# Kernel optimization log

Hardware: AMD Instinct MI355X
Metric: run time of the kernel (lower is better)

Reference implementation:

```python
import jax, jax.numpy as jnp
import numpy as np

NUM_CAMS = 1
NUM_HEADS = 1
NUM_LEVELS = 1
NUM_POINTS = 4
NUM_DEPTH = 128
EMBED = 128  # must equal NUM_DEPTH (output_proj is applied to the depth axis)


def setup_inputs() -> dict:
    key0 = jax.random.key(0)
    ks = jax.random.split(key0, 12)
    bsv, nq, nv = 1, 1024, 1024  # nq == nv == H*W (32*32)
    off_dim = NUM_CAMS * NUM_HEADS * NUM_LEVELS * NUM_DEPTH * NUM_POINTS * 2  # 1024
    aw_dim = NUM_CAMS * NUM_HEADS * NUM_LEVELS * NUM_DEPTH * NUM_POINTS       # 512
    return {
        "query": jax.random.normal(ks[0], (bsv, nq, EMBED), jnp.float32),
        "key": jax.random.normal(ks[1], (NUM_CAMS, nv, bsv, EMBED), jnp.float32),
        "value": jax.random.normal(ks[2], (NUM_CAMS, nv, bsv, EMBED), jnp.float32),
        "ref_3d": jax.random.uniform(ks[3], (bsv * NUM_CAMS, nq * NUM_DEPTH, 2), jnp.float32),
        "spatial_shapes": jnp.array([[32, 32]], dtype=jnp.int32),
        "W_off": jax.random.normal(ks[4], (EMBED, off_dim), jnp.float32) * 0.02,
        "b_off": jax.random.normal(ks[5], (off_dim,), jnp.float32) * 0.02,
        "W_attn": jax.random.normal(ks[6], (EMBED, aw_dim), jnp.float32) * 0.02,
        "b_attn": jax.random.normal(ks[7], (aw_dim,), jnp.float32) * 0.02,
        "W_v": jax.random.normal(ks[8], (EMBED, EMBED), jnp.float32) / np.sqrt(EMBED),
        "b_v": jnp.zeros((EMBED,), jnp.float32),
        "W_o": jax.random.normal(ks[9], (EMBED, EMBED), jnp.float32) / np.sqrt(EMBED),
        "b_o": jnp.zeros((EMBED,), jnp.float32),
    }


def _bilinear_sample(val, H, W, x, y):
    """grid_sample(align_corners=False, padding=zeros) equivalent.
    val: [B, H*W, D]; x, y: [B, Q, P] in pixel coords. Returns [B, Q, P, D]."""
    B, Q, P = x.shape
    D = val.shape[-1]
    x0f = jnp.floor(x); y0f = jnp.floor(y)
    ix0 = x0f.astype(jnp.int32); iy0 = y0f.astype(jnp.int32)
    wx1 = x - x0f; wy1 = y - y0f
    wx0 = 1.0 - wx1; wy0 = 1.0 - wy1

    def corner(ix, iy, w):
        valid = (ix >= 0) & (ix < W) & (iy >= 0) & (iy < H)
        idx = jnp.clip(iy, 0, H - 1) * W + jnp.clip(ix, 0, W - 1)  # [B,Q,P]
        g = jnp.take_along_axis(val, idx.reshape(B, Q * P)[:, :, None], axis=1)
        g = g.reshape(B, Q, P, D)
        return g * (w * valid.astype(val.dtype))[..., None]

    return (corner(ix0, iy0, wx0 * wy0)
            + corner(ix0 + 1, iy0, wx1 * wy0)
            + corner(ix0, iy0 + 1, wx0 * wy1)
            + corner(ix0 + 1, iy0 + 1, wx1 * wy1))


def reference(query, key, value, ref_3d, spatial_shapes,
              W_off, b_off, W_attn, b_attn, W_v, b_v, W_o, b_o):
    bsv, nq, E = query.shape
    cams, nv, bs, _ = key.shape
    identity = query

    # key/value: [cams, nv, bs, E] -> [bsv, nv, E]
    key2 = jnp.transpose(key, (2, 0, 1, 3)).reshape(bsv, nv, E)
    val = jnp.flip(value, axis=0)
    val = jnp.transpose(val, (2, 0, 1, 3)).reshape(bsv, nv, E)
    val = val @ W_v + b_v
    val = val.reshape(bsv * cams, nv, E)  # num_heads=1 -> head_dim=E

    # offsets / attention weights (heads=levels=1 axes squeezed)
    off = (query @ W_off + b_off).reshape(bsv, nq, cams, NUM_DEPTH, NUM_POINTS, 2)
    aw = (query @ W_attn + b_attn).reshape(bsv, nq, cams, NUM_DEPTH, NUM_LEVELS * NUM_POINTS)
    aw = jax.nn.softmax(aw, axis=-1).reshape(bsv, nq, cams, NUM_DEPTH, NUM_POINTS)
    off = jnp.transpose(off, (0, 2, 1, 3, 4, 5)).reshape(bsv * cams, nq * NUM_DEPTH, NUM_POINTS, 2)
    aw = jnp.transpose(aw, (0, 2, 1, 3, 4)).reshape(bsv * cams, nq * NUM_DEPTH, NUM_POINTS)

    H = spatial_shapes[0, 0]
    W = spatial_shapes[0, 1]
    norm = jnp.stack([W, H]).astype(off.dtype)  # [W, H]
    loc = ref_3d[:, :, None, :] + off / norm    # [B, Qe, P, 2] in [0,1]
    x = loc[..., 0] * W.astype(loc.dtype) - 0.5
    y = loc[..., 1] * H.astype(loc.dtype) - 0.5

    sampled = _bilinear_sample(val, H, W, x, y)          # [B, Qe, P, E]
    out = jnp.einsum('bqpe,bqp->bqe', sampled, aw)       # weighted sum over points

    out = out.reshape(bsv, cams, nq, NUM_DEPTH, E).mean(axis=1)  # [bsv, nq, depth, E]
    out = (out * key2[:, :, None, :]).mean(axis=-1)              # [bsv, nq, depth]
    out = out @ W_o + b_o                                        # depth == EMBED
    return out + identity  # dropout = identity in eval
```

## Files before the change

kernel.cpp:

```cpp
#include <hip/hip_runtime.h>


#define NQ   1024
#define NV   1024
#define ND   128
#define NP   4
#define IMG_W 32
#define IMG_H 32
#define QB   4

typedef __attribute__((ext_vector_type(8))) short bfx8;
typedef __attribute__((ext_vector_type(4))) float f32x4;
typedef __attribute__((ext_vector_type(8))) float f32x8;

__device__ __forceinline__ unsigned short bf_rne(float f) {
  unsigned u = __float_as_uint(f);
  return (unsigned short)((u + 0x7FFFu + ((u >> 16) & 1u)) >> 16);
}
__device__ __forceinline__ float bf2f(unsigned short u) {
  return __uint_as_float((unsigned)u << 16);
}
__device__ __forceinline__ bfx8 pack8(const float* p) {
  bfx8 v;
#pragma unroll
  for (int j = 0; j < 8; ++j) v[j] = (short)bf_rne(p[j]);
  return v;
}

__global__ __launch_bounds__(512) void mono_kernel(
    const float* __restrict__ query, const float* __restrict__ key,
    const float* __restrict__ value, const float* __restrict__ ref3d,
    const float* __restrict__ W_off, const float* __restrict__ b_off,
    const float* __restrict__ W_attn, const float* __restrict__ b_attn,
    const float* __restrict__ W_v, const float* __restrict__ b_v,
    const float* __restrict__ W_o, const float* __restrict__ b_o,
    float* __restrict__ out) {
  __shared__ float q_lds[QB][128];
  __shared__ float key_lds[QB][128];
  __shared__ float keyp_lds[QB][128];
  __shared__ float c_lds[QB];
  __shared__ unsigned short img_bf[QB][NV];
  __shared__ unsigned short off_bf[QB][1024];
  __shared__ unsigned short aw_bf[QB][512];
  __shared__ float o1s[QB][128];

  const int tid = threadIdx.x;
  const int q0 = blockIdx.x * QB;
  const int w = tid >> 6, l = tid & 63;
  const int col = l & 15, g = l >> 4;

  if (tid < 128) {
    ((float4*)q_lds)[tid] = ((const float4*)(query + (size_t)q0 * 128))[tid];
  } else if (tid < 256) {
    ((float4*)key_lds)[tid - 128] =
        ((const float4*)(key + (size_t)q0 * 128))[tid - 128];
  }
  __syncthreads();

  {
    bfx8 afK[4];
#pragma unroll
    for (int ks = 0; ks < 4; ++ks) {
      bfx8 a;
      if (col < QB) {
        a = pack8(&key_lds[col][ks * 32 + g * 8]);
      } else {
#pragma unroll
        for (int j = 0; j < 8; ++j) a[j] = 0;
      }
      afK[ks] = a;
    }
    {
      const float* wvp = W_v + (size_t)(w * 16 + col) * 128 + g * 8;
      f32x8 raw[4];
#pragma unroll
      for (int ks = 0; ks < 4; ++ks)
        raw[ks] = *(const f32x8*)(wvp + ks * 32);
      f32x4 acc = {0.f, 0.f, 0.f, 0.f};
#pragma unroll
      for (int ks = 0; ks < 4; ++ks) {
        bfx8 b;
#pragma unroll
        for (int j = 0; j < 8; ++j) b[j] = (short)bf_rne(raw[ks][j]);
        acc = __builtin_amdgcn_mfma_f32_16x16x32_bf16(afK[ks], b, acc,
                                                      0, 0, 0);
      }
      if (g == 0) {
#pragma unroll
        for (int i = 0; i < QB; ++i) keyp_lds[i][w * 16 + col] = acc[i];
      }
    }
    if (tid < QB) {
      float s = 0.f;
      for (int e = 0; e < 128; e += 4) {
        const float4 bv = *(const float4*)(b_v + e);
        const float4 k4 = *(const float4*)(&key_lds[tid][e]);
        s = fmaf(bv.x, k4.x,
            fmaf(bv.y, k4.y, fmaf(bv.z, k4.z, fmaf(bv.w, k4.w, s))));
      }
      c_lds[tid] = s;
    }
  }
  __syncthreads();

  if (w < 4) {
    const int t = tid;
    float4 aoff[QB];
    float2 aaw[QB];
#pragma unroll
    for (int qq = 0; qq < QB; ++qq) {
      aoff[qq] = make_float4(0.f, 0.f, 0.f, 0.f);
      aaw[qq] = make_float2(0.f, 0.f);
    }
    const float* wo_p = W_off + (size_t)t * 4;
    const float* wa_p = W_attn + (size_t)t * 2;
#pragma unroll 8
    for (int e4 = 0; e4 < 32; ++e4) {
      float4 q4[QB];
#pragma unroll
      for (int qq = 0; qq < QB; ++qq)
        q4[qq] = *(const float4*)(&q_lds[qq][e4 * 4]);
#pragma unroll
      for (int j = 0; j < 4; ++j) {
        const int e = e4 * 4 + j;
        const float4 w4 = *(const float4*)(wo_p + (size_t)e * 1024);
        const float2 w2 = *(const float2*)(wa_p + (size_t)e * 512);
#pragma unroll
        for (int qq = 0; qq < QB; ++qq) {
          const float* qp = (const float*)&q4[qq];
          const float qv = qp[j];
          aoff[qq].x = fmaf(qv, w4.x, aoff[qq].x);
          aoff[qq].y = fmaf(qv, w4.y, aoff[qq].y);
          aoff[qq].z = fmaf(qv, w4.z, aoff[qq].z);
          aoff[qq].w = fmaf(qv, w4.w, aoff[qq].w);
          aaw[qq].x = fmaf(qv, w2.x, aaw[qq].x);
          aaw[qq].y = fmaf(qv, w2.y, aaw[qq].y);
        }
      }
    }
    const float4 bo4 = *(const float4*)(b_off + t * 4);
    const float2 ba2 = *(const float2*)(b_attn + t * 2);
#pragma unroll
    for (int qq = 0; qq < QB; ++qq) {
      const unsigned lo = (unsigned)bf_rne(aoff[qq].x + bo4.x) |
                          ((unsigned)bf_rne(aoff[qq].y + bo4.y) << 16);
      const unsigned hi = (unsigned)bf_rne(aoff[qq].z + bo4.z) |
                          ((unsigned)bf_rne(aoff[qq].w + bo4.w) << 16);
      *(uint2*)(&off_bf[qq][t * 4]) = make_uint2(lo, hi);
      *(unsigned*)(&aw_bf[qq][t * 2]) =
          (unsigned)bf_rne(aaw[qq].x + ba2.x) |
          ((unsigned)bf_rne(aaw[qq].y + ba2.y) << 16);
    }
  } else {
    const int ww = w - 4;
    bfx8 afrag[4];
#pragma unroll
    for (int ks = 0; ks < 4; ++ks) {
      bfx8 a;
      if (col < QB) {
        a = pack8(&keyp_lds[col][ks * 32 + g * 8]);
      } else {
#pragma unroll
        for (int j = 0; j < 8; ++j) a[j] = 0;
      }
      afrag[ks] = a;
    }
    float cq[QB];
#pragma unroll
    for (int i = 0; i < QB; ++i) cq[i] = c_lds[i];

    const float* rowp = value + (size_t)(ww * 256 + col) * 128 + g * 8;
#pragma unroll 2
    for (int f = 0; f < 16; ++f) {
      const float* rp = rowp + (size_t)f * 16 * 128;
      f32x8 raw[4];
#pragma unroll
      for (int ks = 0; ks < 4; ++ks)
        raw[ks] = *(const f32x8*)(rp + ks * 32);
      f32x4 acc = {0.f, 0.f, 0.f, 0.f};
#pragma unroll
      for (int ks = 0; ks < 4; ++ks) {
        bfx8 b;
#pragma unroll
        for (int j = 0; j < 8; ++j) b[j] = (short)bf_rne(raw[ks][j]);
        acc = __builtin_amdgcn_mfma_f32_16x16x32_bf16(afrag[ks], b, acc,
                                                      0, 0, 0);
      }
      if (g == 0) {
        const int v = ww * 256 + f * 16 + col;
#pragma unroll
        for (int i = 0; i < QB; ++i)
          img_bf[i][v] = bf_rne(acc[i] + cq[i]);
      }
    }
  }
  __syncthreads();

  {
    const int qq = tid >> 7;
    const int q = q0 + qq;
    const int d = tid & 127;
    const unsigned short* im = img_bf[qq];
    const size_t qe = (size_t)q * ND + d;

    const float rx = ref3d[qe * 2 + 0];
    const float ry = ref3d[qe * 2 + 1];

    const uint2 ua = *(const uint2*)(&aw_bf[qq][d * 4]);
    const float a0 = bf2f((unsigned short)(ua.x & 0xffff));
    const float a1 = bf2f((unsigned short)(ua.x >> 16));
    const float a2 = bf2f((unsigned short)(ua.y & 0xffff));
    const float a3 = bf2f((unsigned short)(ua.y >> 16));
    const float mx = fmaxf(fmaxf(a0, a1), fmaxf(a2, a3));
    const float e0 = __expf(a0 - mx), e1 = __expf(a1 - mx),
                e2 = __expf(a2 - mx), e3 = __expf(a3 - mx);
    const float inv = 1.0f / (e0 + e1 + e2 + e3);
    const float wgt4[4] = {e0 * inv, e1 * inv, e2 * inv, e3 * inv};

    const uint4 uo = *(const uint4*)(&off_bf[qq][d * 8]);
    const unsigned ox[4] = {uo.x, uo.y, uo.z, uo.w};

    float acc = 0.0f;
#pragma unroll
    for (int p = 0; p < NP; ++p) {
      const float x = rx * (float)IMG_W + bf2f((unsigned short)(ox[p] & 0xffff)) - 0.5f;
      const float y = ry * (float)IMG_H + bf2f((unsigned short)(ox[p] >> 16)) - 0.5f;
      const float xf = floorf(x), yf = floorf(y);
      const int ix0 = (int)xf, iy0 = (int)yf;
      const float wx1 = x - xf, wy1 = y - yf;
      const float wx0 = 1.0f - wx1, wy0 = 1.0f - wy1;

      float s = 0.0f;
#pragma unroll
      for (int cy = 0; cy < 2; ++cy) {
#pragma unroll
        for (int cx = 0; cx < 2; ++cx) {
          const int ix = ix0 + cx, iy = iy0 + cy;
          const bool valid = (ix >= 0) & (ix < IMG_W) & (iy >= 0) & (iy < IMG_H);
          const int cix = min(max(ix, 0), IMG_W - 1);
          const int ciy = min(max(iy, 0), IMG_H - 1);
          const float wgt = (cx ? wx1 : wx0) * (cy ? wy1 : wy0);
          s += valid ? bf2f(im[ciy * IMG_W + cix]) * wgt : 0.0f;
        }
      }
      acc += wgt4[p] * s;
    }
    o1s[qq][d] = acc * (1.0f / 128.0f);
  }
  __syncthreads();

  {
    const int qq = tid >> 7;
    const int n = tid & 127;
    float acc = b_o[n] + q_lds[qq][n];
#pragma unroll 8
    for (int d = 0; d < 128; ++d)
      acc = fmaf(o1s[qq][d], W_o[(size_t)d * 128 + n], acc);
    out[(size_t)(q0 + qq) * 128 + n] = acc;
  }
}

extern "C" void kernel_launch(void* const* d_in, const int* in_sizes, int n_in,
                              void* d_out, int out_size, void* d_ws, size_t ws_size,
                              hipStream_t stream) {
  const float* query  = (const float*)d_in[0];
  const float* key    = (const float*)d_in[1];
  const float* value  = (const float*)d_in[2];
  const float* ref3d  = (const float*)d_in[3];
  const float* W_off  = (const float*)d_in[5];
  const float* b_off  = (const float*)d_in[6];
  const float* W_attn = (const float*)d_in[7];
  const float* b_attn = (const float*)d_in[8];
  const float* W_v    = (const float*)d_in[9];
  const float* b_v    = (const float*)d_in[10];
  const float* W_o    = (const float*)d_in[11];
  const float* b_o    = (const float*)d_in[12];
  float* out = (float*)d_out;

  mono_kernel<<<NQ / QB, 512, 0, stream>>>(query, key, value, ref3d,
                                           W_off, b_off, W_attn, b_attn,
                                           W_v, b_v, W_o, b_o, out);
}
```

Before: 121.3 us.

## Pre-convert value and W_v to swizzled bf16 workspace and software-pipeline loads

A new prep kernel converts value and W_v to bf16 once per call into a workspace with an XOR-swizzled row layout. The main kernel then reads half-size bf16 fragments directly instead of loading fp32 and converting in every block, which removes 256x redundant conversion work and halves global traffic. The offset/attention projection and value-projection loops are also software-pipelined with double-buffered register loads, and launch bounds now request two blocks per CU. The cost is an extra kernel launch and workspace round trip, plus higher register pressure from the double buffers.

```diff
diff --git a/kernel.cpp b/kernel.cpp
--- a/kernel.cpp
+++ b/kernel.cpp
@@ -1,4 +1,5 @@
 #include <hip/hip_runtime.h>
+#include <hip/hip_bf16.h>
 
 
 #define NQ   1024
@@ -9,13 +10,16 @@
 #define IMG_H 32
 #define QB   4
 
+#define WS_VAL 0
+#define WS_WV  262144
+
 typedef __attribute__((ext_vector_type(8))) short bfx8;
 typedef __attribute__((ext_vector_type(4))) float f32x4;
-typedef __attribute__((ext_vector_type(8))) float f32x8;
 
 __device__ __forceinline__ unsigned short bf_rne(float f) {
-  unsigned u = __float_as_uint(f);
-  return (unsigned short)((u + 0x7FFFu + ((u >> 16) & 1u)) >> 16);
+  union { __hip_bfloat16 h; unsigned short u; } v;
+  v.h = __float2bfloat16(f);
+  return v.u;
 }
 __device__ __forceinline__ float bf2f(unsigned short u) {
   return __uint_as_float((unsigned)u << 16);
@@ -27,14 +31,83 @@
   return v;
 }
 
-__global__ __launch_bounds__(512) void mono_kernel(
+__global__ __launch_bounds__(256) void prep_kernel(
+    const float* __restrict__ value, const float* __restrict__ W_v,
+    char* __restrict__ ws) {
+  const int idx = blockIdx.x * 256 + threadIdx.x;
+  if (idx < 16384) {
+    const int row = idx >> 4, cc = idx & 15;
+    const bfx8 v = pack8(value + (size_t)row * 128 + cc * 8);
+    *(bfx8*)(ws + WS_VAL + row * 256 + ((cc * 16) ^ ((row & 15) << 4))) = v;
+  } else if (idx < 18432) {
+    const int j = idx - 16384;
+    const int row = j >> 4, cc = j & 15;
+    const bfx8 v = pack8(W_v + (size_t)row * 128 + cc * 8);
+    *(bfx8*)(ws + WS_WV + row * 256 + ((cc * 16) ^ ((row & 15) << 4))) = v;
+  }
+}
+
+#define SLOAD(WO, WA, bb)                                                \
+  _Pragma("unroll") for (int j_ = 0; j_ < 4; ++j_) {                     \
+    WO[j_] = *(const float4*)(wo_p + (size_t)((bb) * 4 + j_) * 1024);    \
+    WA[j_] = *(const float2*)(wa_p + (size_t)((bb) * 4 + j_) * 512);     \
+  }
+
+#define SFMA(WO, WA, bb)                                                 \
+  _Pragma("unroll") for (int j_ = 0; j_ < 4; ++j_) {                     \
+    const int e_ = (bb) * 4 + j_;                                        \
+    _Pragma("unroll") for (int qq_ = 0; qq_ < QB; ++qq_) {               \
+      const float qv_ = q_lds[qq_][e_];                                  \
+      aoff[qq_].x = fmaf(qv_, WO[j_].x, aoff[qq_].x);                    \
+      aoff[qq_].y = fmaf(qv_, WO[j_].y, aoff[qq_].y);                    \
+      aoff[qq_].z = fmaf(qv_, WO[j_].z, aoff[qq_].z);                    \
+      aoff[qq_].w = fmaf(qv_, WO[j_].w, aoff[qq_].w);                    \
+      aaw[qq_].x = fmaf(qv_, WA[j_].x, aaw[qq_].x);                      \
+      aaw[qq_].y = fmaf(qv_, WA[j_].y, aaw[qq_].y);                      \
+    }                                                                    \
+  }
+
+#define VLOAD(D, s_)                                                     \
+  {                                                                      \
+    const char* p_ = lanep + (size_t)(s_) * 8192;                        \
+    D[0] = *(const bfx8*)(p_ + cb0);                                     \
+    D[1] = *(const bfx8*)(p_ + cb1);                                     \
+    D[2] = *(const bfx8*)(p_ + cb2);                                     \
+    D[3] = *(const bfx8*)(p_ + cb3);                                     \
+    D[4] = *(const bfx8*)(p_ + 4096 + cb0);                              \
+    D[5] = *(const bfx8*)(p_ + 4096 + cb1);                              \
+    D[6] = *(const bfx8*)(p_ + 4096 + cb2);                              \
+    D[7] = *(const bfx8*)(p_ + 4096 + cb3);                              \
+  }
+
+#define VCOMP(S, s_)                                                     \
+  {                                                                      \
+    f32x4 a0_ = {0.f, 0.f, 0.f, 0.f}, a1_ = {0.f, 0.f, 0.f, 0.f};       \
+    a0_ = __builtin_amdgcn_mfma_f32_16x16x32_bf16(afrag[0], S[0], a0_, 0, 0, 0); \
+    a0_ = __builtin_amdgcn_mfma_f32_16x16x32_bf16(afrag[1], S[1], a0_, 0, 0, 0); \
+    a0_ = __builtin_amdgcn_mfma_f32_16x16x32_bf16(afrag[2], S[2], a0_, 0, 0, 0); \
+    a0_ = __builtin_amdgcn_mfma_f32_16x16x32_bf16(afrag[3], S[3], a0_, 0, 0, 0); \
+    a1_ = __builtin_amdgcn_mfma_f32_16x16x32_bf16(afrag[0], S[4], a1_, 0, 0, 0); \
+    a1_ = __builtin_amdgcn_mfma_f32_16x16x32_bf16(afrag[1], S[5], a1_, 0, 0, 0); \
+    a1_ = __builtin_amdgcn_mfma_f32_16x16x32_bf16(afrag[2], S[6], a1_, 0, 0, 0); \
+    a1_ = __builtin_amdgcn_mfma_f32_16x16x32_bf16(afrag[3], S[7], a1_, 0, 0, 0); \
+    if (g == 0) {                                                        \
+      const int v_ = ww * 256 + (s_) * 32 + col;                         \
+      _Pragma("unroll") for (int i_ = 0; i_ < QB; ++i_) {                \
+        img_bf[i_][v_] = bf_rne(a0_[i_] + cq[i_]);                       \
+        img_bf[i_][v_ + 16] = bf_rne(a1_[i_] + cq[i_]);                  \
+      }                                                                  \
+    }                                                                    \
+  }
+
+__global__ __launch_bounds__(512, 2) void mono_kernel(
     const float* __restrict__ query, const float* __restrict__ key,
-    const float* __restrict__ value, const float* __restrict__ ref3d,
+    const float* __restrict__ ref3d,
     const float* __restrict__ W_off, const float* __restrict__ b_off,
     const float* __restrict__ W_attn, const float* __restrict__ b_attn,
-    const float* __restrict__ W_v, const float* __restrict__ b_v,
+    const float* __restrict__ b_v,
     const float* __restrict__ W_o, const float* __restrict__ b_o,
-    float* __restrict__ out) {
+    const char* __restrict__ ws, float* __restrict__ out) {
   __shared__ float q_lds[QB][128];
   __shared__ float key_lds[QB][128];
   __shared__ float keyp_lds[QB][128];
@@ -49,6 +122,14 @@
   const int w = tid >> 6, l = tid & 63;
   const int col = l & 15, g = l >> 4;
 
+  const int cb0 = (0 + g * 16) ^ (col << 4);
+  const int cb1 = (64 + g * 16) ^ (col << 4);
+  const int cb2 = (128 + g * 16) ^ (col << 4);
+  const int cb3 = (192 + g * 16) ^ (col << 4);
+
+  const char* wsval = ws + WS_VAL;
+  const char* wswv = ws + WS_WV;
+
   if (tid < 128) {
     ((float4*)q_lds)[tid] = ((const float4*)(query + (size_t)q0 * 128))[tid];
   } else if (tid < 256) {
@@ -71,20 +152,16 @@
       afK[ks] = a;
     }
     {
-      const float* wvp = W_v + (size_t)(w * 16 + col) * 128 + g * 8;
-      f32x8 raw[4];
-#pragma unroll
-      for (int ks = 0; ks < 4; ++ks)
-        raw[ks] = *(const f32x8*)(wvp + ks * 32);
+      const char* kvp = wswv + (size_t)(w * 16 + col) * 256;
+      const bfx8 b0 = *(const bfx8*)(kvp + cb0);
+      const bfx8 b1 = *(const bfx8*)(kvp + cb1);
+      const bfx8 b2 = *(const bfx8*)(kvp + cb2);
+      const bfx8 b3 = *(const bfx8*)(kvp + cb3);
       f32x4 acc = {0.f, 0.f, 0.f, 0.f};
-#pragma unroll
-      for (int ks = 0; ks < 4; ++ks) {
-        bfx8 b;
-#pragma unroll
-        for (int j = 0; j < 8; ++j) b[j] = (short)bf_rne(raw[ks][j]);
-        acc = __builtin_amdgcn_mfma_f32_16x16x32_bf16(afK[ks], b, acc,
-                                                      0, 0, 0);
-      }
+      acc = __builtin_amdgcn_mfma_f32_16x16x32_bf16(afK[0], b0, acc, 0, 0, 0);
+      acc = __builtin_amdgcn_mfma_f32_16x16x32_bf16(afK[1], b1, acc, 0, 0, 0);
+      acc = __builtin_amdgcn_mfma_f32_16x16x32_bf16(afK[2], b2, acc, 0, 0, 0);
+      acc = __builtin_amdgcn_mfma_f32_16x16x32_bf16(afK[3], b3, acc, 0, 0, 0);
       if (g == 0) {
 #pragma unroll
         for (int i = 0; i < QB; ++i) keyp_lds[i][w * 16 + col] = acc[i];
@@ -114,30 +191,17 @@
     }
     const float* wo_p = W_off + (size_t)t * 4;
     const float* wa_p = W_attn + (size_t)t * 2;
-#pragma unroll 8
-    for (int e4 = 0; e4 < 32; ++e4) {
-      float4 q4[QB];
-#pragma unroll
-      for (int qq = 0; qq < QB; ++qq)
-        q4[qq] = *(const float4*)(&q_lds[qq][e4 * 4]);
-#pragma unroll
-      for (int j = 0; j < 4; ++j) {
-        const int e = e4 * 4 + j;
-        const float4 w4 = *(const float4*)(wo_p + (size_t)e * 1024);
-        const float2 w2 = *(const float2*)(wa_p + (size_t)e * 512);
-#pragma unroll
-        for (int qq = 0; qq < QB; ++qq) {
-          const float* qp = (const float*)&q4[qq];
-          const float qv = qp[j];
-          aoff[qq].x = fmaf(qv, w4.x, aoff[qq].x);
-          aoff[qq].y = fmaf(qv, w4.y, aoff[qq].y);
-          aoff[qq].z = fmaf(qv, w4.z, aoff[qq].z);
-          aoff[qq].w = fmaf(qv, w4.w, aoff[qq].w);
-          aaw[qq].x = fmaf(qv, w2.x, aaw[qq].x);
-          aaw[qq].y = fmaf(qv, w2.y, aaw[qq].y);
-        }
-      }
-    }
+
+    float4 woA[4], woB[4];
+    float2 waA[4], waB[4];
+    SLOAD(woA, waA, 0);
+    for (int b = 0; b < 32; b += 2) {
+      SLOAD(woB, waB, b + 1);
+      SFMA(woA, waA, b);
+      if (b + 2 < 32) SLOAD(woA, waA, b + 2);
+      SFMA(woB, waB, b + 1);
+    }
+
     const float4 bo4 = *(const float4*)(b_off + t * 4);
     const float2 ba2 = *(const float2*)(b_attn + t * 2);
 #pragma unroll
@@ -169,29 +233,14 @@
 #pragma unroll
     for (int i = 0; i < QB; ++i) cq[i] = c_lds[i];
 
-    const float* rowp = value + (size_t)(ww * 256 + col) * 128 + g * 8;
-#pragma unroll 2
-    for (int f = 0; f < 16; ++f) {
-      const float* rp = rowp + (size_t)f * 16 * 128;
-      f32x8 raw[4];
-#pragma unroll
-      for (int ks = 0; ks < 4; ++ks)
-        raw[ks] = *(const f32x8*)(rp + ks * 32);
-      f32x4 acc = {0.f, 0.f, 0.f, 0.f};
-#pragma unroll
-      for (int ks = 0; ks < 4; ++ks) {
-        bfx8 b;
-#pragma unroll
-        for (int j = 0; j < 8; ++j) b[j] = (short)bf_rne(raw[ks][j]);
-        acc = __builtin_amdgcn_mfma_f32_16x16x32_bf16(afrag[ks], b, acc,
-                                                      0, 0, 0);
-      }
-      if (g == 0) {
-        const int v = ww * 256 + f * 16 + col;
-#pragma unroll
-        for (int i = 0; i < QB; ++i)
-          img_bf[i][v] = bf_rne(acc[i] + cq[i]);
-      }
+    const char* lanep = wsval + ((size_t)ww * 256 + col) * 256;
+    bfx8 vA[8], vB[8];
+    VLOAD(vA, 0);
+    for (int s = 0; s < 8; s += 2) {
+      VLOAD(vB, s + 1);
+      VCOMP(vA, s);
+      if (s + 2 < 8) VLOAD(vA, s + 2);
+      VCOMP(vB, s + 1);
     }
   }
   __syncthreads();
@@ -276,8 +325,10 @@
   const float* W_o    = (const float*)d_in[11];
   const float* b_o    = (const float*)d_in[12];
   float* out = (float*)d_out;
-
-  mono_kernel<<<NQ / QB, 512, 0, stream>>>(query, key, value, ref3d,
+  char* ws = (char*)d_ws;
+
+  prep_kernel<<<72, 256, 0, stream>>>(value, W_v, ws);
+  mono_kernel<<<NQ / QB, 512, 0, stream>>>(query, key, ref3d,
                                            W_off, b_off, W_attn, b_attn,
-                                           W_v, b_v, W_o, b_o, out);
-}
+                                           b_v, W_o, b_o, ws, out);
+}
```

Result: faster. 101.2 us (-16.6%).
